# Performance work log

Measured on AMD Instinct MI355X. Metric: run time of the kernel, lower is better.

Reference implementation:

```python
import jax, jax.numpy as jnp
import numpy as np

DIM = 1024
HEADS = 8
DIM_HEAD = 64
INNER = HEADS * DIM_HEAD  # 512
B, N = 2, 2048
SCALE = DIM_HEAD ** -0.5
EPS = 1e-5


def layer_norm(x, gamma):
    # lucidrains LayerNorm: learned gamma, fixed zero beta
    mu = jnp.mean(x, axis=-1, keepdims=True)
    var = jnp.var(x, axis=-1, keepdims=True)
    return (x - mu) * jax.lax.rsqrt(var + EPS) * gamma


def setup_inputs() -> dict:
    key = jax.random.key(0)
    ks = jax.random.split(key, 8)
    x = jax.random.normal(ks[0], (B, N, DIM), dtype=jnp.float32)
    mask = jax.random.randint(ks[1], (B, N), 0, 2) > 0  # bool padding mask
    attn_bias = jax.random.normal(ks[2], (HEADS, N, N), dtype=jnp.float32)
    gamma = jnp.ones((DIM,), dtype=jnp.float32)
    s = 0.02
    Wq = jax.random.normal(ks[3], (DIM, INNER), dtype=jnp.float32) * s
    Wkv = jax.random.normal(ks[4], (DIM, 2 * DIM_HEAD), dtype=jnp.float32) * s
    Wo = jax.random.normal(ks[5], (INNER, DIM), dtype=jnp.float32) * s
    return {"x": x, "mask": mask, "attn_bias": attn_bias, "gamma": gamma,
            "Wq": Wq, "Wkv": Wkv, "Wo": Wo}


def reference(x, mask, attn_bias, gamma, Wq, Wkv, Wo):
    b, n, _ = x.shape
    kv_input = x  # NOTE: K/V use the UN-normalized input (per source ordering)
    xn = layer_norm(x, gamma)
    q = xn @ Wq                       # [b, n, inner]
    kv = kv_input @ Wkv               # [b, n, 2*dh]
    k, v = jnp.split(kv, 2, axis=-1)  # each [b, n, dh] (single shared KV head)
    q = q.reshape(b, n, HEADS, DIM_HEAD).transpose(0, 2, 1, 3) * SCALE  # [b,h,n,dh]
    sim = jnp.einsum('bhid,bjd->bhij', q, k)
    sim = sim + attn_bias             # attn_bias [h,i,j] broadcasts over batch
    neg = -jnp.finfo(sim.dtype).max
    sim = jnp.where(mask[:, None, None, :], sim, neg)
    causal_mask = jnp.triu(jnp.ones((n, n), dtype=bool), k=1)
    sim = jnp.where(causal_mask, neg, sim)
    attn = jax.nn.softmax(sim, axis=-1)
    out = jnp.einsum('bhij,bjd->bhid', attn, v)          # [b,h,n,dh]
    out = out.transpose(0, 2, 1, 3).reshape(b, n, INNER)  # [b,n,inner]
    return out @ Wo
```

## Files before the change

kernel.cpp:

```cpp
#include <hip/hip_runtime.h>
#include <cfloat>
#include <cstdint>
#include <cstddef>

#define N_TOK 2048
#define D_MODEL 1024
#define N_HEAD 8
#define D_HEAD 64
#define N_BATCH 2
#define INNER_DIM 512

typedef __attribute__((ext_vector_type(4))) float f32x4;
typedef __bf16 bfv8 __attribute__((ext_vector_type(8)));

#define KEEPV(x) asm volatile("" : : "v"(x))

__device__ __forceinline__ short f2bf(float f) {
  union { float f; unsigned u; } x{f};
  unsigned r = (x.u + 0x7fffu + ((x.u >> 16) & 1u)) >> 16;
  return (short)r;
}
__device__ __forceinline__ float bf2f(short s) {
  union { unsigned u; float f; } x;
  x.u = ((unsigned)(unsigned short)s) << 16;
  return x.f;
}
__device__ __forceinline__ void gload_lds16(const void* g, void* l) {
  __builtin_amdgcn_global_load_lds(
      (const __attribute__((address_space(1))) void*)g,
      (__attribute__((address_space(3))) void*)l, 16, 0, 0);
}

__global__ __launch_bounds__(256) void ln_cast_kernel(
    const float* __restrict__ x, const float* __restrict__ gamma,
    short* __restrict__ xn, short* __restrict__ xb) {
  const int row = blockIdx.x;
  const int tid = threadIdx.x;
  const float4 v = ((const float4*)(x + (size_t)row * D_MODEL))[tid];
  float s = v.x + v.y + v.z + v.w;
  float s2 = v.x * v.x + v.y * v.y + v.z * v.z + v.w * v.w;
#pragma unroll
  for (int off = 1; off < 64; off <<= 1) {
    s += __shfl_xor(s, off);
    s2 += __shfl_xor(s2, off);
  }
  __shared__ float red[8];
  const int wid = tid >> 6;
  if ((tid & 63) == 0) { red[wid] = s; red[wid + 4] = s2; }
  __syncthreads();
  s = red[0] + red[1] + red[2] + red[3];
  s2 = red[4] + red[5] + red[6] + red[7];
  const float mu = s * (1.f / D_MODEL);
  const float var = s2 * (1.f / D_MODEL) - mu * mu;
  const float rstd = rsqrtf(var + 1e-5f);
  const float4 g = ((const float4*)gamma)[tid];
  short4 xnv, xbv;
  xnv.x = f2bf((v.x - mu) * rstd * g.x);
  xnv.y = f2bf((v.y - mu) * rstd * g.y);
  xnv.z = f2bf((v.z - mu) * rstd * g.z);
  xnv.w = f2bf((v.w - mu) * rstd * g.w);
  xbv.x = f2bf(v.x); xbv.y = f2bf(v.y); xbv.z = f2bf(v.z); xbv.w = f2bf(v.w);
  ((short4*)(xn + (size_t)row * D_MODEL))[tid] = xnv;
  ((short4*)(xb + (size_t)row * D_MODEL))[tid] = xbv;
}

__global__ __launch_bounds__(256) void wcast_all_kernel(
    const float* __restrict__ Wq, const float* __restrict__ Wkv,
    const float* __restrict__ Wo, short* __restrict__ wqt,
    short* __restrict__ wkvt, short* __restrict__ wot) {
  const int bid = blockIdx.x;
  const float* W; short* Wt; int K, Nc, n0, k0;
  if (bid < 128) {
    W = Wq; Wt = wqt; K = 1024; Nc = 512;
    n0 = (bid & 7) * 64; k0 = (bid >> 3) * 64;
  } else if (bid < 160) {
    const int t = bid - 128;
    W = Wkv; Wt = wkvt; K = 1024; Nc = 128;
    n0 = (t & 1) * 64; k0 = (t >> 1) * 64;
  } else {
    const int t = bid - 160;
    W = Wo; Wt = wot; K = 512; Nc = 1024;
    n0 = (t & 15) * 64; k0 = (t >> 4) * 64;
  }
  __shared__ short t[64][65];
  const int tid = threadIdx.x;
#pragma unroll
  for (int i = 0; i < 16; ++i) {
    int lin = i * 256 + tid;
    int kr = lin >> 6, nc = lin & 63;
    t[nc][kr] = f2bf(W[(size_t)(k0 + kr) * Nc + n0 + nc]);
  }
  __syncthreads();
#pragma unroll
  for (int i = 0; i < 16; ++i) {
    int lin = i * 256 + tid;
    int nr = lin >> 6, kc = lin & 63;
    Wt[(size_t)(n0 + nr) * K + k0 + kc] = t[nr][kc];
  }
}

__global__ __launch_bounds__(256) void qkv_gemm_kernel(
    const short* __restrict__ xn, const short* __restrict__ xb,
    const short* __restrict__ wqt, const short* __restrict__ wkvt,
    short* __restrict__ q, short* __restrict__ kb, short* __restrict__ vt) {
  const bool isQ = blockIdx.x < 8;
  const short* A = isQ ? xn : xb;
  const short* Bt = isQ ? wqt : wkvt;
  const int n0 = (isQ ? blockIdx.x : (blockIdx.x - 8)) * 64;
  const int m0 = blockIdx.y * 128;
  const int K = 1024;
  __shared__ __align__(16) short As[128 * 64];
  __shared__ __align__(16) short Bs[64 * 64];
  const int tid = threadIdx.x;
  const int lane = tid & 63, wid = tid >> 6;
  const int l15 = lane & 15, l4 = lane >> 4;
  const int wr = wid * 32;
  f32x4 acc[2][4] = {};
  for (int k0 = 0; k0 < K; k0 += 64) {
#pragma unroll
    for (int it = 0; it < 4; ++it) {
      int c = it * 256 + tid;
      int r = c >> 3, cc = (c & 7) << 3;
      gload_lds16(A + (size_t)(m0 + r) * K + k0 + cc, As + (size_t)(it * 256 + wid * 64) * 8);
    }
#pragma unroll
    for (int it = 0; it < 2; ++it) {
      int c = it * 256 + tid;
      int r = c >> 3, cc = (c & 7) << 3;
      gload_lds16(Bt + (size_t)(n0 + r) * K + k0 + cc, Bs + (size_t)(it * 256 + wid * 64) * 8);
    }
    __syncthreads();
#pragma unroll
    for (int kk = 0; kk < 2; ++kk) {
      bfv8 af[2], bfr[4];
#pragma unroll
      for (int i = 0; i < 2; ++i)
        af[i] = *(const bfv8*)&As[(wr + i * 16 + l15) * 64 + kk * 32 + l4 * 8];
#pragma unroll
      for (int i = 0; i < 4; ++i)
        bfr[i] = *(const bfv8*)&Bs[(i * 16 + l15) * 64 + kk * 32 + l4 * 8];
#pragma unroll
      for (int mi = 0; mi < 2; ++mi)
#pragma unroll
        for (int ni = 0; ni < 4; ++ni)
          acc[mi][ni] = __builtin_amdgcn_mfma_f32_16x16x32_bf16(af[mi], bfr[ni], acc[mi][ni], 0, 0, 0);
    }
    __syncthreads();
  }
#pragma unroll
  for (int mi = 0; mi < 2; ++mi) {
#pragma unroll
    for (int ni = 0; ni < 4; ++ni) {
#pragma unroll
      for (int r = 0; r < 4; ++r) {
        const int row = m0 + wr + mi * 16 + l4 * 4 + r;
        const int col = n0 + ni * 16 + l15;
        const float v = acc[mi][ni][r];
        const int b = row >> 11, n = row & (N_TOK - 1);
        if (isQ) {
          const int h = col >> 6, d = col & 63;
          q[(((size_t)(b * N_HEAD + h)) * N_TOK + n) * D_HEAD + d] = f2bf(v * 0.125f);
        } else {
          if (col < 64)
            kb[((size_t)b * N_TOK + n) * D_HEAD + col] = f2bf(v);
          else
            vt[((size_t)b * D_HEAD + (col - 64)) * N_TOK + n] = f2bf(v);
        }
      }
    }
  }
}

__global__ __launch_bounds__(256) void ogemm_kernel(
    const short* __restrict__ A, const short* __restrict__ Bt,
    float* __restrict__ C, int M, int N, int K) {
  __shared__ __align__(16) short As[128 * 64];
  __shared__ __align__(16) short Bs[128 * 64];
  const int tid = threadIdx.x;
  const int lane = tid & 63, wid = tid >> 6;
  const int l15 = lane & 15, l4 = lane >> 4;
  const int m0 = blockIdx.y * 128, n0 = blockIdx.x * 128;
  const int wr = (wid >> 1) * 64, wc = (wid & 1) * 64;
  f32x4 acc[4][4] = {};
  for (int k0 = 0; k0 < K; k0 += 64) {
#pragma unroll
    for (int it = 0; it < 4; ++it) {
      int c = it * 256 + tid;
      int r = c >> 3, cc = (c & 7) << 3;
      gload_lds16(A + (size_t)(m0 + r) * K + k0 + cc, As + (size_t)(it * 256 + wid * 64) * 8);
      gload_lds16(Bt + (size_t)(n0 + r) * K + k0 + cc, Bs + (size_t)(it * 256 + wid * 64) * 8);
    }
    __syncthreads();
#pragma unroll
    for (int kk = 0; kk < 2; ++kk) {
      bfv8 af[4], bfr[4];
#pragma unroll
      for (int i = 0; i < 4; ++i) {
        af[i] = *(const bfv8*)&As[(wr + i * 16 + l15) * 64 + kk * 32 + l4 * 8];
        bfr[i] = *(const bfv8*)&Bs[(wc + i * 16 + l15) * 64 + kk * 32 + l4 * 8];
      }
#pragma unroll
      for (int mi = 0; mi < 4; ++mi)
#pragma unroll
        for (int ni = 0; ni < 4; ++ni)
          acc[mi][ni] = __builtin_amdgcn_mfma_f32_16x16x32_bf16(af[mi], bfr[ni], acc[mi][ni], 0, 0, 0);
    }
    __syncthreads();
  }
#pragma unroll
  for (int mi = 0; mi < 4; ++mi)
#pragma unroll
    for (int ni = 0; ni < 4; ++ni)
#pragma unroll
      for (int r = 0; r < 4; ++r) {
        const int row = m0 + wr + mi * 16 + l4 * 4 + r;
        const int col = n0 + wc + ni * 16 + l15;
        C[(size_t)row * N + col] = acc[mi][ni][r];
      }
}

__global__ __launch_bounds__(256) void vmean_kernel(const short* __restrict__ vt,
                                                    float* __restrict__ vm) {
  const int bd = blockIdx.x;
  const short* rowp = vt + (size_t)bd * N_TOK;
  const int tid = threadIdx.x;
  float s = 0.f;
  for (int i = tid; i < N_TOK; i += 256) s += bf2f(rowp[i]);
#pragma unroll
  for (int off = 1; off < 64; off <<= 1) s += __shfl_xor(s, off);
  __shared__ float red[4];
  if ((tid & 63) == 0) red[tid >> 6] = s;
  __syncthreads();
  if (tid == 0) vm[bd] = (red[0] + red[1] + red[2] + red[3]) * (1.f / N_TOK);
}

__global__ __launch_bounds__(64, 2) void attn_kernel(
    const short* __restrict__ qg,
    const short* __restrict__ kg,
    const short* __restrict__ vtg,
    const float* __restrict__ bias,
    const int* __restrict__ mask,
    const float* __restrict__ vm,
    short* __restrict__ og) {
  const int bh = blockIdx.x;
  const int qw = 127 - (int)blockIdx.y;
  const int b = bh >> 3, h = bh & 7;
  const int lane = threadIdx.x;
  const int l15 = lane & 15, l4 = lane >> 4;

  __shared__ __align__(16) short plds[1024];

  const int qrow0 = qw * 16;
  const short* qp = qg + ((size_t)bh * N_TOK + qrow0 + l15) * D_HEAD + l4 * 8;
  const bfv8 qf0 = *(const bfv8*)qp;
  const bfv8 qf1 = *(const bfv8*)(qp + 32);
  const int i_base = qrow0 + l4 * 4;
  const int nt = qw / 8 + 1;

  f32x4 oacc[4] = {};
  float m_r[4], l_r[4];
#pragma unroll
  for (int r = 0; r < 4; ++r) { m_r[r] = -FLT_MAX; l_r[r] = 0.f; }

  const float* bias_base = bias + ((size_t)h * N_TOK + i_base) * N_TOK + l15;
  const int* mask_b = mask + b * N_TOK + l15;

  float bX[32], bY[32];
#pragma unroll
  for (int mf = 0; mf < 8; ++mf)
#pragma unroll
    for (int r = 0; r < 4; ++r)
      bX[mf * 4 + r] = bias_base[(size_t)r * N_TOK + mf * 16];

  int t = 0;
#define BODY(BC, BN)                                                                    \
  {                                                                                     \
    const int j0 = t * 128;                                                             \
    int mk[8];                                                                          \
    _Pragma("unroll") for (int mf = 0; mf < 8; ++mf) mk[mf] = mask_b[j0 + mf * 16];     \
    bfv8 vf[16];                                                                        \
    const short* vp = vtg + ((size_t)b * D_HEAD + l15) * N_TOK + j0 + l4 * 8;           \
    _Pragma("unroll") for (int hh = 0; hh < 2; ++hh)                                    \
        _Pragma("unroll") for (int ks = 0; ks < 2; ++ks)                                \
            _Pragma("unroll") for (int df = 0; df < 4; ++df)                            \
                vf[hh * 8 + ks * 4 + df] =                                              \
                    *(const bfv8*)(vp + hh * 64 + df * (16 * N_TOK) + ks * 32);         \
    f32x4 s[8] = {};                                                                    \
    const short* kp = kg + ((size_t)b * N_TOK + j0 + l15) * D_HEAD + l4 * 8;            \
    _Pragma("unroll") for (int ks = 0; ks < 2; ++ks) {                                  \
      const bfv8 qf = ks ? qf1 : qf0;                                                   \
      _Pragma("unroll") for (int mf = 0; mf < 8; ++mf) {                                \
        const bfv8 kf = *(const bfv8*)(kp + mf * (16 * D_HEAD) + ks * 32);              \
        s[mf] = __builtin_amdgcn_mfma_f32_16x16x32_bf16(qf, kf, s[mf], 0, 0, 0);        \
      }                                                                                 \
    }                                                                                   \
          \
    _Pragma("unroll") for (int mf = 0; mf < 8; ++mf) KEEPV(mk[mf]);                     \
    _Pragma("unroll") for (int i = 0; i < 16; ++i) KEEPV(vf[i]);                        \
    __builtin_amdgcn_sched_barrier(0);                                                  \
    {                                                                                   \
      const int jn = (t + 1 < nt) ? (t + 1) * 128 : j0;                                 \
      _Pragma("unroll") for (int mf = 0; mf < 8; ++mf)                                  \
          _Pragma("unroll") for (int r = 0; r < 4; ++r)                                 \
              BN[mf * 4 + r] = bias_base[(size_t)r * N_TOK + jn + mf * 16];             \
    }                                                                                   \
    __builtin_amdgcn_sched_barrier(0);                                                  \
    float rowmax[4] = {-FLT_MAX, -FLT_MAX, -FLT_MAX, -FLT_MAX};                         \
    _Pragma("unroll") for (int mf = 0; mf < 8; ++mf) {                                  \
      const int j = j0 + mf * 16 + l15;                                                 \
      _Pragma("unroll") for (int r = 0; r < 4; ++r) {                                   \
        float v = s[mf][r] + BC[mf * 4 + r];                                            \
        const bool ok = (j <= i_base + r) && (mk[mf] != 0);                             \
        v = ok ? v : -FLT_MAX;                                                          \
        s[mf][r] = v;                                                                   \
        rowmax[r] = fmaxf(rowmax[r], v);                                                \
      }                                                                                 \
    }                                                                                   \
    _Pragma("unroll") for (int off = 1; off < 16; off <<= 1)                            \
        _Pragma("unroll") for (int r = 0; r < 4; ++r)                                   \
            rowmax[r] = fmaxf(rowmax[r], __shfl_xor(rowmax[r], off));                   \
    float alpha[4], rsum[4];                                                            \
    _Pragma("unroll") for (int r = 0; r < 4; ++r) {                                     \
      const float mn = fmaxf(m_r[r], rowmax[r]);                                        \
      alpha[r] = __expf(m_r[r] - mn);                                                   \
      m_r[r] = mn;                                                                      \
      float rs = 0.f;                                                                   \
      _Pragma("unroll") for (int mf = 0; mf < 8; ++mf) {                                \
        const float e = __expf(s[mf][r] - mn);                                          \
        s[mf][r] = e;                                                                   \
        rs += e;                                                                        \
      }                                                                                 \
      rsum[r] = rs;                                                                     \
    }                                                                                   \
    _Pragma("unroll") for (int off = 1; off < 16; off <<= 1)                            \
        _Pragma("unroll") for (int r = 0; r < 4; ++r)                                   \
            rsum[r] += __shfl_xor(rsum[r], off);                                        \
    _Pragma("unroll") for (int r = 0; r < 4; ++r)                                       \
        l_r[r] = l_r[r] * alpha[r] + rsum[r];                                           \
    _Pragma("unroll") for (int df = 0; df < 4; ++df)                                    \
        _Pragma("unroll") for (int r = 0; r < 4; ++r)                                   \
            oacc[df][r] *= alpha[r];                                                    \
    _Pragma("unroll") for (int hh = 0; hh < 2; ++hh) {                                  \
      _Pragma("unroll") for (int nf = 0; nf < 4; ++nf) {                                \
        const int ch = (nf * 16 + l15) >> 3;                                            \
        const int cl = l15 & 7;                                                         \
        _Pragma("unroll") for (int r = 0; r < 4; ++r) {                                 \
          const int row = l4 * 4 + r;                                                   \
          const int g = row * 8 + (ch ^ (row & 7));                                     \
          plds[g * 8 + cl] = f2bf(s[hh * 4 + nf][r]);                                   \
        }                                                                               \
      }                                                                                 \
      _Pragma("unroll") for (int ks = 0; ks < 2; ++ks) {                                \
        const int g = l15 * 8 + ((ks * 4 + l4) ^ (l15 & 7));                            \
        const bfv8 pf = *(const bfv8*)&plds[g * 8];                                     \
        _Pragma("unroll") for (int df = 0; df < 4; ++df)                                \
          oacc[df] = __builtin_amdgcn_mfma_f32_16x16x32_bf16(                           \
              pf, vf[hh * 8 + ks * 4 + df], oacc[df], 0, 0, 0);                         \
      }                                                                                 \
    }                                                                                   \
    ++t;                                                                                \
  }

  while (t < nt) {
    BODY(bX, bY)
    if (t >= nt) break;
    BODY(bY, bX)
  }
#undef BODY

#pragma unroll
  for (int r = 0; r < 4; ++r) {
    const int i = i_base + r;
    const bool degen = (m_r[r] == -FLT_MAX);
    const float sc = degen ? 0.f : 1.f / l_r[r];
#pragma unroll
    for (int df = 0; df < 4; ++df) {
      const int d = df * 16 + l15;
      float v = oacc[df][r] * sc;
      if (degen) v = vm[b * D_HEAD + d];
      og[((size_t)b * N_TOK + i) * INNER_DIM + h * D_HEAD + d] = f2bf(v);
    }
  }
}

extern "C" void kernel_launch(void* const* d_in, const int* in_sizes, int n_in,
                              void* d_out, int out_size, void* d_ws, size_t ws_size,
                              hipStream_t stream) {
  const float* x = (const float*)d_in[0];
  const int* mask = (const int*)d_in[1];
  const float* bias = (const float*)d_in[2];
  const float* gamma = (const float*)d_in[3];
  const float* Wq = (const float*)d_in[4];
  const float* Wkv = (const float*)d_in[5];
  const float* Wo = (const float*)d_in[6];
  float* out = (float*)d_out;

  char* w = (char*)d_ws;
  short* xn = (short*)w;  w += (size_t)4096 * 1024 * 2;
  short* xb = (short*)w;  w += (size_t)4096 * 1024 * 2;
  short* wqt = (short*)w; w += (size_t)512 * 1024 * 2;
  short* wkvt = (short*)w; w += (size_t)128 * 1024 * 2;
  short* wot = (short*)w; w += (size_t)1024 * 512 * 2;
  short* q = (short*)w;   w += (size_t)16 * 2048 * 64 * 2;
  short* kb = (short*)w;  w += (size_t)2 * 2048 * 64 * 2;
  short* vt = (short*)w;  w += (size_t)2 * 64 * 2048 * 2;
  short* og = (short*)w;  w += (size_t)4096 * 512 * 2;
  float* vm = (float*)w;  w += 128 * 4;

  ln_cast_kernel<<<4096, 256, 0, stream>>>(x, gamma, xn, xb);
  wcast_all_kernel<<<288, 256, 0, stream>>>(Wq, Wkv, Wo, wqt, wkvt, wot);
  qkv_gemm_kernel<<<dim3(10, 32), 256, 0, stream>>>(xn, xb, wqt, wkvt, q, kb, vt);
  vmean_kernel<<<128, 256, 0, stream>>>(vt, vm);
  attn_kernel<<<dim3(16, 128), 64, 0, stream>>>(q, kb, vt, bias, mask, vm, og);
  ogemm_kernel<<<dim3(8, 32), 256, 0, stream>>>(og, wot, out, 4096, 1024, 512);
}
```

Measured before the change: 139.4 us.

## Transpose attention MFMA layout so each lane owns one query row

Swaps the MFMA operand order so the score tile is computed transposed, giving each lane a single query row with 4 consecutive key columns. This lets bias and mask be loaded as 16-byte vectors instead of scalar strided loads, and reduces the row max and sum shuffles to two cross-group xor steps. P is written to LDS as packed bf16 pairs with a new XOR swizzle, V is loaded in a matching order, and the output is stored as short4 vectors. It carries some risk of LDS bank conflicts or numerical mismatch if the new swizzle or layout mapping is wrong.

Result: slower. 149.2 us (+7.1%).

```diff
diff --git a/kernel.cpp b/kernel.cpp
--- a/kernel.cpp
+++ b/kernel.cpp
@@ -11,6 +11,7 @@
 #define INNER_DIM 512
 
 typedef __attribute__((ext_vector_type(4))) float f32x4;
+typedef __attribute__((ext_vector_type(4))) int i32x4;
 typedef __bf16 bfv8 __attribute__((ext_vector_type(8)));
 
 #define KEEPV(x) asm volatile("" : : "v"(x))
@@ -248,115 +249,106 @@
   const int lane = threadIdx.x;
   const int l15 = lane & 15, l4 = lane >> 4;
 
-  __shared__ __align__(16) short plds[1024];
+  __shared__ __align__(16) short plds[16 * 128];
+  unsigned* plds_u = (unsigned*)plds;
 
   const int qrow0 = qw * 16;
   const short* qp = qg + ((size_t)bh * N_TOK + qrow0 + l15) * D_HEAD + l4 * 8;
   const bfv8 qf0 = *(const bfv8*)qp;
   const bfv8 qf1 = *(const bfv8*)(qp + 32);
-  const int i_base = qrow0 + l4 * 4;
+  const int i_q = qrow0 + l15;
   const int nt = qw / 8 + 1;
 
   f32x4 oacc[4] = {};
-  float m_r[4], l_r[4];
-#pragma unroll
-  for (int r = 0; r < 4; ++r) { m_r[r] = -FLT_MAX; l_r[r] = 0.f; }
-
-  const float* bias_base = bias + ((size_t)h * N_TOK + i_base) * N_TOK + l15;
-  const int* mask_b = mask + b * N_TOK + l15;
-
-  float bX[32], bY[32];
+  float m_s = -FLT_MAX, l_s = 0.f;
+
+  const float* bias_row = bias + ((size_t)h * N_TOK + i_q) * N_TOK;
+  const int* mask_b2 = mask + b * N_TOK;
+  const int xsw = (l15 & 3) << 4;
+
+  f32x4 bX[8], bY[8];
 #pragma unroll
   for (int mf = 0; mf < 8; ++mf)
-#pragma unroll
-    for (int r = 0; r < 4; ++r)
-      bX[mf * 4 + r] = bias_base[(size_t)r * N_TOK + mf * 16];
+    bX[mf] = *(const f32x4*)&bias_row[mf * 16 + l4 * 4];
 
   int t = 0;
 #define BODY(BC, BN)                                                                    \
   {                                                                                     \
     const int j0 = t * 128;                                                             \
-    int mk[8];                                                                          \
-    _Pragma("unroll") for (int mf = 0; mf < 8; ++mf) mk[mf] = mask_b[j0 + mf * 16];     \
+    i32x4 mi[8];                                                                        \
+    _Pragma("unroll") for (int mf = 0; mf < 8; ++mf)                                    \
+        mi[mf] = *(const i32x4*)&mask_b2[j0 + mf * 16 + l4 * 4];                        \
     bfv8 vf[16];                                                                        \
     const short* vp = vtg + ((size_t)b * D_HEAD + l15) * N_TOK + j0 + l4 * 8;           \
-    _Pragma("unroll") for (int hh = 0; hh < 2; ++hh)                                    \
-        _Pragma("unroll") for (int ks = 0; ks < 2; ++ks)                                \
-            _Pragma("unroll") for (int df = 0; df < 4; ++df)                            \
-                vf[hh * 8 + ks * 4 + df] =                                              \
-                    *(const bfv8*)(vp + hh * 64 + df * (16 * N_TOK) + ks * 32);         \
-    f32x4 s[8] = {};                                                                    \
+    _Pragma("unroll") for (int js = 0; js < 4; ++js)                                    \
+        _Pragma("unroll") for (int df = 0; df < 4; ++df)                                \
+            vf[js * 4 + df] = *(const bfv8*)(vp + js * 32 + df * (16 * N_TOK));         \
+    f32x4 s2[8] = {};                                                                   \
     const short* kp = kg + ((size_t)b * N_TOK + j0 + l15) * D_HEAD + l4 * 8;            \
     _Pragma("unroll") for (int ks = 0; ks < 2; ++ks) {                                  \
       const bfv8 qf = ks ? qf1 : qf0;                                                   \
       _Pragma("unroll") for (int mf = 0; mf < 8; ++mf) {                                \
         const bfv8 kf = *(const bfv8*)(kp + mf * (16 * D_HEAD) + ks * 32);              \
-        s[mf] = __builtin_amdgcn_mfma_f32_16x16x32_bf16(qf, kf, s[mf], 0, 0, 0);        \
+        s2[mf] = __builtin_amdgcn_mfma_f32_16x16x32_bf16(kf, qf, s2[mf], 0, 0, 0);      \
       }                                                                                 \
     }                                                                                   \
-          \
-    _Pragma("unroll") for (int mf = 0; mf < 8; ++mf) KEEPV(mk[mf]);                     \
-    _Pragma("unroll") for (int i = 0; i < 16; ++i) KEEPV(vf[i]);                        \
     __builtin_amdgcn_sched_barrier(0);                                                  \
     {                                                                                   \
       const int jn = (t + 1 < nt) ? (t + 1) * 128 : j0;                                 \
       _Pragma("unroll") for (int mf = 0; mf < 8; ++mf)                                  \
-          _Pragma("unroll") for (int r = 0; r < 4; ++r)                                 \
-              BN[mf * 4 + r] = bias_base[(size_t)r * N_TOK + jn + mf * 16];             \
+          BN[mf] = *(const f32x4*)&bias_row[jn + mf * 16 + l4 * 4];                     \
     }                                                                                   \
     __builtin_amdgcn_sched_barrier(0);                                                  \
-    float rowmax[4] = {-FLT_MAX, -FLT_MAX, -FLT_MAX, -FLT_MAX};                         \
+                                                     \
     _Pragma("unroll") for (int mf = 0; mf < 8; ++mf) {                                  \
-      const int j = j0 + mf * 16 + l15;                                                 \
       _Pragma("unroll") for (int r = 0; r < 4; ++r) {                                   \
-        float v = s[mf][r] + BC[mf * 4 + r];                                            \
-        const bool ok = (j <= i_base + r) && (mk[mf] != 0);                             \
-        v = ok ? v : -FLT_MAX;                                                          \
-        s[mf][r] = v;                                                                   \
-        rowmax[r] = fmaxf(rowmax[r], v);                                                \
+        const int j = j0 + mf * 16 + l4 * 4 + r;                                        \
+        float v = s2[mf][r] + BC[mf][r];                                                \
+        const bool ok = (j <= i_q) && (mi[mf][r] != 0);                                 \
+        s2[mf][r] = ok ? v : -FLT_MAX;                                                  \
       }                                                                                 \
     }                                                                                   \
-    _Pragma("unroll") for (int off = 1; off < 16; off <<= 1)                            \
-        _Pragma("unroll") for (int r = 0; r < 4; ++r)                                   \
-            rowmax[r] = fmaxf(rowmax[r], __shfl_xor(rowmax[r], off));                   \
-    float alpha[4], rsum[4];                                                            \
+                                                 \
+    f32x4 mx4;                                                                          \
     _Pragma("unroll") for (int r = 0; r < 4; ++r) {                                     \
-      const float mn = fmaxf(m_r[r], rowmax[r]);                                        \
-      alpha[r] = __expf(m_r[r] - mn);                                                   \
-      m_r[r] = mn;                                                                      \
-      float rs = 0.f;                                                                   \
-      _Pragma("unroll") for (int mf = 0; mf < 8; ++mf) {                                \
-        const float e = __expf(s[mf][r] - mn);                                          \
-        s[mf][r] = e;                                                                   \
-        rs += e;                                                                        \
+      float a0 = fmaxf(s2[0][r], s2[1][r]), a1 = fmaxf(s2[2][r], s2[3][r]);             \
+      float a2 = fmaxf(s2[4][r], s2[5][r]), a3 = fmaxf(s2[6][r], s2[7][r]);             \
+      mx4[r] = fmaxf(fmaxf(a0, a1), fmaxf(a2, a3));                                     \
+    }                                                                                   \
+    float pm = fmaxf(fmaxf(mx4[0], mx4[1]), fmaxf(mx4[2], mx4[3]));                     \
+    pm = fmaxf(pm, __shfl_xor(pm, 16));                                                 \
+    pm = fmaxf(pm, __shfl_xor(pm, 32));                                                 \
+    const float mn = fmaxf(m_s, pm);                                                    \
+    const float alpha = __expf(m_s - mn);                                               \
+    m_s = mn;                                                                           \
+    float rs = 0.f;                                                                     \
+    _Pragma("unroll") for (int mf = 0; mf < 8; ++mf)                                    \
+        _Pragma("unroll") for (int r = 0; r < 4; ++r) {                                 \
+          const float e = __expf(s2[mf][r] - mn);                                       \
+          s2[mf][r] = e;                                                                \
+          rs += e;                                                                      \
+        }                                                                               \
+    rs += __shfl_xor(rs, 16);                                                           \
+    rs += __shfl_xor(rs, 32);                                                           \
+    l_s = l_s * alpha + rs;                                                             \
+    _Pragma("unroll") for (int df = 0; df < 4; ++df)                                    \
+        _Pragma("unroll") for (int r = 0; r < 4; ++r) oacc[df][r] *= alpha;             \
+                                       \
+    _Pragma("unroll") for (int mf = 0; mf < 8; ++mf) {                                  \
+      _Pragma("unroll") for (int rp = 0; rp < 2; ++rp) {                                \
+        const unsigned lo = (unsigned short)f2bf(s2[mf][rp * 2]);                       \
+        const unsigned hi = (unsigned short)f2bf(s2[mf][rp * 2 + 1]);                   \
+        const int jj = (mf * 16 + l4 * 4 + rp * 2) ^ xsw;                               \
+        plds_u[l15 * 64 + (jj >> 1)] = lo | (hi << 16);                                 \
       }                                                                                 \
-      rsum[r] = rs;                                                                     \
-    }                                                                                   \
-    _Pragma("unroll") for (int off = 1; off < 16; off <<= 1)                            \
-        _Pragma("unroll") for (int r = 0; r < 4; ++r)                                   \
-            rsum[r] += __shfl_xor(rsum[r], off);                                        \
-    _Pragma("unroll") for (int r = 0; r < 4; ++r)                                       \
-        l_r[r] = l_r[r] * alpha[r] + rsum[r];                                           \
-    _Pragma("unroll") for (int df = 0; df < 4; ++df)                                    \
-        _Pragma("unroll") for (int r = 0; r < 4; ++r)                                   \
-            oacc[df][r] *= alpha[r];                                                    \
-    _Pragma("unroll") for (int hh = 0; hh < 2; ++hh) {                                  \
-      _Pragma("unroll") for (int nf = 0; nf < 4; ++nf) {                                \
-        const int ch = (nf * 16 + l15) >> 3;                                            \
-        const int cl = l15 & 7;                                                         \
-        _Pragma("unroll") for (int r = 0; r < 4; ++r) {                                 \
-          const int row = l4 * 4 + r;                                                   \
-          const int g = row * 8 + (ch ^ (row & 7));                                     \
-          plds[g * 8 + cl] = f2bf(s[hh * 4 + nf][r]);                                   \
-        }                                                                               \
-      }                                                                                 \
-      _Pragma("unroll") for (int ks = 0; ks < 2; ++ks) {                                \
-        const int g = l15 * 8 + ((ks * 4 + l4) ^ (l15 & 7));                            \
-        const bfv8 pf = *(const bfv8*)&plds[g * 8];                                     \
-        _Pragma("unroll") for (int df = 0; df < 4; ++df)                                \
+    }                                                                                   \
+                                            \
+    _Pragma("unroll") for (int js = 0; js < 4; ++js) {                                  \
+      const int jj = (js * 32 + l4 * 8) ^ xsw;                                          \
+      const bfv8 pf = *(const bfv8*)&plds[l15 * 128 + jj];                              \
+      _Pragma("unroll") for (int df = 0; df < 4; ++df)                                  \
           oacc[df] = __builtin_amdgcn_mfma_f32_16x16x32_bf16(                           \
-              pf, vf[hh * 8 + ks * 4 + df], oacc[df], 0, 0, 0);                         \
-      }                                                                                 \
+              vf[js * 4 + df], pf, oacc[df], 0, 0, 0);                                  \
     }                                                                                   \
     ++t;                                                                                \
   }
@@ -368,18 +360,19 @@
   }
 #undef BODY
 
-#pragma unroll
-  for (int r = 0; r < 4; ++r) {
-    const int i = i_base + r;
-    const bool degen = (m_r[r] == -FLT_MAX);
-    const float sc = degen ? 0.f : 1.f / l_r[r];
-#pragma unroll
-    for (int df = 0; df < 4; ++df) {
-      const int d = df * 16 + l15;
+  const bool degen = (m_s == -FLT_MAX);
+  const float sc = degen ? 0.f : 1.f / l_s;
+#pragma unroll
+  for (int df = 0; df < 4; ++df) {
+    const f32x4 vm4 = *(const f32x4*)&vm[b * D_HEAD + df * 16 + l4 * 4];
+    short4 o4;
+#pragma unroll
+    for (int r = 0; r < 4; ++r) {
       float v = oacc[df][r] * sc;
-      if (degen) v = vm[b * D_HEAD + d];
-      og[((size_t)b * N_TOK + i) * INNER_DIM + h * D_HEAD + d] = f2bf(v);
-    }
+      if (degen) v = vm4[r];
+      ((short*)&o4)[r] = f2bf(v);
+    }
+    *(short4*)&og[((size_t)b * N_TOK + i_q) * INNER_DIM + h * D_HEAD + df * 16 + l4 * 4] = o4;
   }
 }
 
```

## Split attention KV tiles across two blocks and merge with a combine kernel

Applied to the files above, without the earlier changes.

The attention grid gains a z dimension of 2. Each block handles every other 128-key tile and writes an unnormalized partial output plus its per-row max and sum. A new combine kernel merges the two partials with a log-sum-exp rescale and handles fully masked rows by writing the V mean. This doubles the number of blocks and evens out the causal load imbalance, at the cost of an extra launch and a bf16 round-trip of the partials through the workspace. The workspace is reused for this, in buffers that are dead by that point. The launch bounds also rise to 4 waves per SIMD, which caps the register budget and may cause spills given the large per-thread bias and V register arrays.

Result: slower. 356.4 us (+155.7%).

```diff
diff --git a/kernel.cpp b/kernel.cpp
--- a/kernel.cpp
+++ b/kernel.cpp
@@ -234,16 +234,17 @@
   if (tid == 0) vm[bd] = (red[0] + red[1] + red[2] + red[3]) * (1.f / N_TOK);
 }
 
-__global__ __launch_bounds__(64, 2) void attn_kernel(
+__global__ __launch_bounds__(64, 4) void attn_kernel(
     const short* __restrict__ qg,
     const short* __restrict__ kg,
     const short* __restrict__ vtg,
     const float* __restrict__ bias,
     const int* __restrict__ mask,
-    const float* __restrict__ vm,
-    short* __restrict__ og) {
+    short* __restrict__ part_o,
+    float* __restrict__ part_ml) {
   const int bh = blockIdx.x;
   const int qw = 127 - (int)blockIdx.y;
+  const int sz = blockIdx.z;
   const int b = bh >> 3, h = bh & 7;
   const int lane = threadIdx.x;
   const int l15 = lane & 15, l4 = lane >> 4;
@@ -266,13 +267,15 @@
   const int* mask_b = mask + b * N_TOK + l15;
 
   float bX[32], bY[32];
-#pragma unroll
-  for (int mf = 0; mf < 8; ++mf)
-#pragma unroll
-    for (int r = 0; r < 4; ++r)
-      bX[mf * 4 + r] = bias_base[(size_t)r * N_TOK + mf * 16];
-
-  int t = 0;
+  if (sz < nt) {
+#pragma unroll
+    for (int mf = 0; mf < 8; ++mf)
+#pragma unroll
+      for (int r = 0; r < 4; ++r)
+        bX[mf * 4 + r] = bias_base[(size_t)r * N_TOK + sz * 128 + mf * 16];
+  }
+
+  int t = sz;
 #define BODY(BC, BN)                                                                    \
   {                                                                                     \
     const int j0 = t * 128;                                                             \
@@ -294,12 +297,11 @@
         s[mf] = __builtin_amdgcn_mfma_f32_16x16x32_bf16(qf, kf, s[mf], 0, 0, 0);        \
       }                                                                                 \
     }                                                                                   \
-          \
     _Pragma("unroll") for (int mf = 0; mf < 8; ++mf) KEEPV(mk[mf]);                     \
     _Pragma("unroll") for (int i = 0; i < 16; ++i) KEEPV(vf[i]);                        \
     __builtin_amdgcn_sched_barrier(0);                                                  \
     {                                                                                   \
-      const int jn = (t + 1 < nt) ? (t + 1) * 128 : j0;                                 \
+      const int jn = (t + 2 < nt) ? (t + 2) * 128 : j0;                                 \
       _Pragma("unroll") for (int mf = 0; mf < 8; ++mf)                                  \
           _Pragma("unroll") for (int r = 0; r < 4; ++r)                                 \
               BN[mf * 4 + r] = bias_base[(size_t)r * N_TOK + jn + mf * 16];             \
@@ -328,7 +330,7 @@
       _Pragma("unroll") for (int mf = 0; mf < 8; ++mf) {                                \
         const float e = __expf(s[mf][r] - mn);                                          \
         s[mf][r] = e;                                                                   \
-        rs += e;                                                                        \
+        rs += e;                                                                       \
       }                                                                                 \
       rsum[r] = rs;                                                                     \
     }                                                                                   \
@@ -358,7 +360,7 @@
               pf, vf[hh * 8 + ks * 4 + df], oacc[df], 0, 0, 0);                         \
       }                                                                                 \
     }                                                                                   \
-    ++t;                                                                                \
+    t += 2;                                                                             \
   }
 
   while (t < nt) {
@@ -368,18 +370,53 @@
   }
 #undef BODY
 
+  const int blk = (bh << 7) + qw;
+  short* po = part_o + ((size_t)blk * 2 + sz) * 1024;
 #pragma unroll
   for (int r = 0; r < 4; ++r) {
-    const int i = i_base + r;
-    const bool degen = (m_r[r] == -FLT_MAX);
-    const float sc = degen ? 0.f : 1.f / l_r[r];
-#pragma unroll
-    for (int df = 0; df < 4; ++df) {
-      const int d = df * 16 + l15;
-      float v = oacc[df][r] * sc;
-      if (degen) v = vm[b * D_HEAD + d];
-      og[((size_t)b * N_TOK + i) * INNER_DIM + h * D_HEAD + d] = f2bf(v);
-    }
+    const int row = l4 * 4 + r;
+#pragma unroll
+    for (int df = 0; df < 4; ++df)
+      po[row * 64 + df * 16 + l15] = f2bf(oacc[df][r]);
+  }
+  if (l15 == 0) {
+    float* pm = part_ml + ((size_t)blk * 2 + sz) * 32;
+#pragma unroll
+    for (int r = 0; r < 4; ++r) {
+      pm[(l4 * 4 + r) * 2] = m_r[r];
+      pm[(l4 * 4 + r) * 2 + 1] = l_r[r];
+    }
+  }
+}
+
+__global__ __launch_bounds__(64) void combine_kernel(
+    const short* __restrict__ part_o, const float* __restrict__ part_ml,
+    const float* __restrict__ vm, short* __restrict__ og) {
+  const int blk = blockIdx.x;
+  const int bh = blk >> 7, qw = blk & 127;
+  const int b = bh >> 3, h = bh & 7;
+  const int lane = threadIdx.x;
+  const short* p0 = part_o + (size_t)blk * 2048;
+  const short* p1 = p0 + 1024;
+  const float* ml0 = part_ml + (size_t)blk * 64;
+  const float* ml1 = ml0 + 32;
+  const float vmd = vm[b * D_HEAD + lane];
+#pragma unroll 4
+  for (int row = 0; row < 16; ++row) {
+    const float m0 = ml0[row * 2], l0 = ml0[row * 2 + 1];
+    const float m1 = ml1[row * 2], l1 = ml1[row * 2 + 1];
+    const float m = fmaxf(m0, m1);
+    float v;
+    if (m == -FLT_MAX) {
+      v = vmd;
+    } else {
+      const float w0 = (m0 > -FLT_MAX) ? __expf(m0 - m) : 0.f;
+      const float w1 = (m1 > -FLT_MAX) ? __expf(m1 - m) : 0.f;
+      const float l = w0 * l0 + w1 * l1;
+      const float o = w0 * bf2f(p0[row * 64 + lane]) + w1 * bf2f(p1[row * 64 + lane]);
+      v = o / l;
+    }
+    og[((size_t)b * N_TOK + qw * 16 + row) * INNER_DIM + h * D_HEAD + lane] = f2bf(v);
   }
 }
 
@@ -407,10 +444,14 @@
   short* og = (short*)w;  w += (size_t)4096 * 512 * 2;
   float* vm = (float*)w;  w += 128 * 4;
 
+  short* part_o = (short*)d_ws;
+  float* part_ml = (float*)((char*)d_ws + (size_t)10 * 1024 * 1024);
+
   ln_cast_kernel<<<4096, 256, 0, stream>>>(x, gamma, xn, xb);
   wcast_all_kernel<<<288, 256, 0, stream>>>(Wq, Wkv, Wo, wqt, wkvt, wot);
   qkv_gemm_kernel<<<dim3(10, 32), 256, 0, stream>>>(xn, xb, wqt, wkvt, q, kb, vt);
   vmean_kernel<<<128, 256, 0, stream>>>(vt, vm);
-  attn_kernel<<<dim3(16, 128), 64, 0, stream>>>(q, kb, vt, bias, mask, vm, og);
+  attn_kernel<<<dim3(16, 128, 2), 64, 0, stream>>>(q, kb, vt, bias, mask, part_o, part_ml);
+  combine_kernel<<<2048, 64, 0, stream>>>(part_o, part_ml, vm, og);
   ogemm_kernel<<<dim3(8, 32), 256, 0, stream>>>(og, wot, out, 4096, 1024, 512);
 }
```
